# Performance work log

Hardware: AMD Instinct MI355X
Metric: run time of the kernel (lower is better)

## Reference

```python
import jax, jax.numpy as jnp
import numpy as np

N_E = 1024
E_DIM = 64
BETA = 0.25


def setup_inputs() -> dict:
    key = jax.random.key(0)
    k1, k2 = jax.random.split(key)
    z = jax.random.normal(k1, (32, 32, 32, E_DIM), dtype=jnp.float32)
    # torch init: uniform(-1/n_e, 1/n_e)
    codebook = jax.random.uniform(k2, (N_E, E_DIM), dtype=jnp.float32,
                                  minval=-1.0 / N_E, maxval=1.0 / N_E)
    return {"z": z, "codebook": codebook}


def reference(z, codebook):
    z_flat = z.reshape(-1, E_DIM)  # [N, e_dim]
    # squared euclidean distances: ||z||^2 + ||e||^2 - 2 z e^T
    d = (jnp.sum(z_flat ** 2, axis=1, keepdims=True)
         + jnp.sum(codebook ** 2, axis=1)
         - 2.0 * jnp.matmul(z_flat, codebook.T))  # [N, n_e]
    idx = jnp.argmin(d, axis=1)  # [N]
    z_q = codebook[idx].reshape(z.shape)
    sg = jax.lax.stop_gradient
    loss = jnp.mean((sg(z_q) - z) ** 2) + BETA * jnp.mean((z_q - sg(z)) ** 2)
    z_q_st = z + sg(z_q - z)  # straight-through estimator
    return z_q_st, idx, loss
```

## Files before the change

kernel.cpp:

```cpp
#include <hip/hip_runtime.h>
#include <hip/hip_bf16.h>

#define NROWS 32768
#define NE    1024
#define ED    64
#define RPB   32
#define RPW   8
#define CHUNK 256

typedef float4 f4;

__global__ __launch_bounds__(256)
void vq_main(const float* __restrict__ z, const float* __restrict__ cb,
             float* __restrict__ out, float* __restrict__ partials)
{
    __shared__ __align__(16) float zsh[RPB * ED];
    __shared__ __align__(16) float et[ED * CHUNK];
    __shared__ __align__(16) float sq[CHUNK];
    __shared__ int   idxsh[RPB];
    __shared__ float wsum[4];

    const int tid  = threadIdx.x;
    const int lane = tid & 63;
    const int w    = tid >> 6;
    const int rowbase = blockIdx.x * RPB;

    {
        const f4* zg = (const f4*)(z + (size_t)rowbase * ED);
        f4* zs = (f4*)zsh;
        zs[tid]       = zg[tid];
        zs[tid + 256] = zg[tid + 256];
    }
    __syncthreads();

    float cn[RPW];
    {
        float rj;
        {
#pragma clang fp contract(off)
            const int rl = lane >> 3;
            const int jj = lane & 7;
            const float* zr = &zsh[(w * RPW + rl) * ED];
            float a = 0.f;
#pragma unroll
            for (int i = 0; i < 8; ++i) { float v = zr[8 * i + jj]; a += v * v; }
            rj = a;
        }
        rj += __shfl_xor(rj, 1);
        rj += __shfl_xor(rj, 2);
        rj += __shfl_xor(rj, 4);
#pragma unroll
        for (int r = 0; r < RPW; ++r) cn[r] = __shfl(rj, r * 8);
    }

    float bestv[RPW];
    int   besti[RPW];
#pragma unroll
    for (int r = 0; r < RPW; ++r) { bestv[r] = INFINITY; besti[r] = 0; }

    const f4* zs4 = (const f4*)zsh;
    const f4* et4 = (const f4*)et;
    const f4* sq4 = (const f4*)sq;

    for (int ch = 0; ch < 4; ++ch) {
        __syncthreads();
        {
            const int code = ch * CHUNK + tid;
            const f4* crow = (const f4*)(cb + (size_t)code * ED);
            float v[ED];
#pragma unroll
            for (int i = 0; i < 16; ++i) {
                f4 t = crow[i];
                v[4 * i + 0] = t.x; v[4 * i + 1] = t.y;
                v[4 * i + 2] = t.z; v[4 * i + 3] = t.w;
            }
            {
#pragma clang fp contract(off)
                float r0 = v[0] * v[0], r1 = v[1] * v[1];
                float r2 = v[2] * v[2], r3 = v[3] * v[3];
                float r4 = v[4] * v[4], r5 = v[5] * v[5];
                float r6 = v[6] * v[6], r7 = v[7] * v[7];
#pragma unroll
                for (int i = 8; i < ED; i += 8) {
                    r0 += v[i + 0] * v[i + 0]; r1 += v[i + 1] * v[i + 1];
                    r2 += v[i + 2] * v[i + 2]; r3 += v[i + 3] * v[i + 3];
                    r4 += v[i + 4] * v[i + 4]; r5 += v[i + 5] * v[i + 5];
                    r6 += v[i + 6] * v[i + 6]; r7 += v[i + 7] * v[i + 7];
                }
                sq[tid] = ((r0 + r1) + (r2 + r3)) + ((r4 + r5) + (r6 + r7));
            }
#pragma unroll
            for (int i = 0; i < ED; ++i) et[i * CHUNK + tid] = v[i];
        }
        __syncthreads();

        f4 sv = sq4[lane];
        float svq[4] = {sv.x, sv.y, sv.z, sv.w};

        float acc[RPW][4];
#pragma unroll
        for (int r = 0; r < RPW; ++r)
            acc[r][0] = acc[r][1] = acc[r][2] = acc[r][3] = 0.f;

#pragma unroll 2
        for (int k4 = 0; k4 < 16; ++k4) {
            f4 e0 = et4[(4 * k4 + 0) * 64 + lane];
            f4 e1 = et4[(4 * k4 + 1) * 64 + lane];
            f4 e2 = et4[(4 * k4 + 2) * 64 + lane];
            f4 e3 = et4[(4 * k4 + 3) * 64 + lane];
#pragma unroll
            for (int r = 0; r < RPW; ++r) {
                f4 zv = zs4[(w * RPW + r) * 16 + k4];
                acc[r][0] = fmaf(zv.x, e0.x, acc[r][0]);
                acc[r][1] = fmaf(zv.x, e0.y, acc[r][1]);
                acc[r][2] = fmaf(zv.x, e0.z, acc[r][2]);
                acc[r][3] = fmaf(zv.x, e0.w, acc[r][3]);
                acc[r][0] = fmaf(zv.y, e1.x, acc[r][0]);
                acc[r][1] = fmaf(zv.y, e1.y, acc[r][1]);
                acc[r][2] = fmaf(zv.y, e1.z, acc[r][2]);
                acc[r][3] = fmaf(zv.y, e1.w, acc[r][3]);
                acc[r][0] = fmaf(zv.z, e2.x, acc[r][0]);
                acc[r][1] = fmaf(zv.z, e2.y, acc[r][1]);
                acc[r][2] = fmaf(zv.z, e2.z, acc[r][2]);
                acc[r][3] = fmaf(zv.z, e2.w, acc[r][3]);
                acc[r][0] = fmaf(zv.w, e3.x, acc[r][0]);
                acc[r][1] = fmaf(zv.w, e3.y, acc[r][1]);
                acc[r][2] = fmaf(zv.w, e3.z, acc[r][2]);
                acc[r][3] = fmaf(zv.w, e3.w, acc[r][3]);
            }
        }

        {
#pragma clang fp contract(off)
#pragma unroll
            for (int r = 0; r < RPW; ++r) {
#pragma unroll
                for (int q = 0; q < 4; ++q) {
                    float t1 = cn[r] + svq[q];
                    float d  = t1 - 2.0f * acc[r][q];
                    int j = ch * 256 + lane * 4 + q;
                    if (d < bestv[r]) { bestv[r] = d; besti[r] = j; }
                }
            }
        }
    }

    float lp = 0.f;
#pragma unroll
    for (int r = 0; r < RPW; ++r) {
        float v = bestv[r];
        int   i = besti[r];
#pragma unroll
        for (int m = 1; m < 64; m <<= 1) {
            float ov = __shfl_xor(v, m);
            int   oi = __shfl_xor(i, m);
            if (ov < v || (ov == v && oi < i)) { v = ov; i = oi; }
        }
        i &= (NE - 1);
        const int grow = rowbase + w * RPW + r;
        float zq, zz, diff, st;
        {
#pragma clang fp contract(off)
            zq   = cb[(size_t)i * ED + lane];
            zz   = zsh[(w * RPW + r) * ED + lane];
            diff = zq - zz;
            st   = zz + diff;
            lp  += diff * diff;
        }
        out[(size_t)grow * ED + lane] = st;
        if (lane == 0) idxsh[w * RPW + r] = i;
    }

#pragma unroll
    for (int m = 1; m < 64; m <<= 1) lp += __shfl_xor(lp, m);
    if (lane == 0) wsum[w] = lp;
    __syncthreads();

    if (tid < RPB) {
        int iv = idxsh[tid] & (NE - 1);
        out[(size_t)NROWS * ED + rowbase + tid] = (float)iv;
    }
    if (tid == 0)
        partials[blockIdx.x] = (wsum[0] + wsum[1]) + (wsum[2] + wsum[3]);
}

__global__ void vq_finalize(const float* __restrict__ partials,
                            float* __restrict__ out)
{
    __shared__ float red[256];
    int t = threadIdx.x;
    float s = (partials[t] + partials[t + 256]) + (partials[t + 512] + partials[t + 768]);
    red[t] = s;
    __syncthreads();
    for (int m = 128; m > 0; m >>= 1) {
        if (t < m) red[t] += red[t + m];
        __syncthreads();
    }
    if (t == 0) {
        float mean = red[0] / (float)((size_t)NROWS * ED);
        float loss = mean + 0.25f * mean;
        out[(size_t)NROWS * ED + NROWS] = loss;
    }
}

extern "C" void kernel_launch(void* const* d_in, const int* in_sizes, int n_in,
                              void* d_out, int out_size, void* d_ws, size_t ws_size,
                              hipStream_t stream)
{
    (void)in_sizes; (void)n_in; (void)out_size; (void)ws_size;
    const float* z  = (const float*)d_in[0];
    const float* cb = (const float*)d_in[1];
    float* out = (float*)d_out;
    float* partials = (float*)d_ws;

    vq_main<<<1024, 256, 0, stream>>>(z, cb, out, partials);
    vq_finalize<<<1, 256, 0, stream>>>(partials, out);
}
```

Measured before the change: 90.16 us.

## Precompute codebook norms in prep kernel and read z rows directly via scalar loads

Moves the codebook squared-norm computation into a small prep kernel run once, instead of recomputing it in each of the 1024 blocks. The main kernel no longer stages z in shared memory. It reads z rows from global memory at wave-uniform addresses, so they can become scalar loads. It also requests two blocks per CU through launch bounds. The cost is an extra kernel launch and the dependence on global or scalar cache for z reads in the inner loop.

```diff
diff --git a/kernel.cpp b/kernel.cpp
--- a/kernel.cpp
+++ b/kernel.cpp
@@ -1,56 +1,74 @@
 #include <hip/hip_runtime.h>
-#include <hip/hip_bf16.h>
 
 #define NROWS 32768
 #define NE    1024
 #define ED    64
-#define RPB   32
+#define CHUNK 256
+#define NCH   (NE / CHUNK)
 #define RPW   8
-#define CHUNK 256
 
 typedef float4 f4;
 
-__global__ __launch_bounds__(256)
+__global__ void vq_prep(const float* __restrict__ cb, float* __restrict__ ssq)
+{
+    int j = blockIdx.x * blockDim.x + threadIdx.x;
+    const f4* crow = (const f4*)(cb + (size_t)j * ED);
+    float v[ED];
+#pragma unroll
+    for (int i = 0; i < 16; ++i) {
+        f4 t = crow[i];
+        v[4*i+0] = t.x; v[4*i+1] = t.y; v[4*i+2] = t.z; v[4*i+3] = t.w;
+    }
+    {
+#pragma clang fp contract(off)
+        float r0 = v[0]*v[0], r1 = v[1]*v[1], r2 = v[2]*v[2], r3 = v[3]*v[3];
+        float r4 = v[4]*v[4], r5 = v[5]*v[5], r6 = v[6]*v[6], r7 = v[7]*v[7];
+#pragma unroll
+        for (int i = 8; i < ED; i += 8) {
+            r0 += v[i+0]*v[i+0]; r1 += v[i+1]*v[i+1];
+            r2 += v[i+2]*v[i+2]; r3 += v[i+3]*v[i+3];
+            r4 += v[i+4]*v[i+4]; r5 += v[i+5]*v[i+5];
+            r6 += v[i+6]*v[i+6]; r7 += v[i+7]*v[i+7];
+        }
+        ssq[j] = ((r0+r1)+(r2+r3)) + ((r4+r5)+(r6+r7));
+    }
+}
+
+__global__ __launch_bounds__(256, 2)
 void vq_main(const float* __restrict__ z, const float* __restrict__ cb,
-             float* __restrict__ out, float* __restrict__ partials)
-{
-    __shared__ __align__(16) float zsh[RPB * ED];
+             const float* __restrict__ ssq, float* __restrict__ out,
+             float* __restrict__ partials)
+{
     __shared__ __align__(16) float et[ED * CHUNK];
-    __shared__ __align__(16) float sq[CHUNK];
-    __shared__ int   idxsh[RPB];
+    __shared__ __align__(16) float sqsh[NE];
+    __shared__ int   idxsh[32];
     __shared__ float wsum[4];
 
     const int tid  = threadIdx.x;
     const int lane = tid & 63;
     const int w    = tid >> 6;
-    const int rowbase = blockIdx.x * RPB;
-
-    {
-        const f4* zg = (const f4*)(z + (size_t)rowbase * ED);
-        f4* zs = (f4*)zsh;
-        zs[tid]       = zg[tid];
-        zs[tid + 256] = zg[tid + 256];
-    }
-    __syncthreads();
+    const int w_u  = __builtin_amdgcn_readfirstlane(w);
+    const int rowbase = blockIdx.x * 32;
+
+    ((f4*)sqsh)[tid] = ((const f4*)ssq)[tid];
 
     float cn[RPW];
     {
-        float rj;
-        {
-#pragma clang fp contract(off)
-            const int rl = lane >> 3;
-            const int jj = lane & 7;
-            const float* zr = &zsh[(w * RPW + rl) * ED];
-            float a = 0.f;
-#pragma unroll
-            for (int i = 0; i < 8; ++i) { float v = zr[8 * i + jj]; a += v * v; }
-            rj = a;
-        }
-        rj += __shfl_xor(rj, 1);
-        rj += __shfl_xor(rj, 2);
-        rj += __shfl_xor(rj, 4);
-#pragma unroll
-        for (int r = 0; r < RPW; ++r) cn[r] = __shfl(rj, r * 8);
+        const int rl = lane >> 3;
+        const int jj = lane & 7;
+        const float* zr = z + (size_t)(rowbase + w_u * RPW + rl) * ED;
+        float a;
+        {
+#pragma clang fp contract(off)
+            a = 0.f;
+#pragma unroll
+            for (int i = 0; i < 8; ++i) { float v = zr[8*i + jj]; a += v*v; }
+        }
+        a += __shfl_xor(a, 1);
+        a += __shfl_xor(a, 2);
+        a += __shfl_xor(a, 4);
+#pragma unroll
+        for (int r = 0; r < RPW; ++r) cn[r] = __shfl(a, r * 8);
     }
 
     float bestv[RPW];
@@ -58,43 +76,25 @@
 #pragma unroll
     for (int r = 0; r < RPW; ++r) { bestv[r] = INFINITY; besti[r] = 0; }
 
-    const f4* zs4 = (const f4*)zsh;
     const f4* et4 = (const f4*)et;
-    const f4* sq4 = (const f4*)sq;
-
-    for (int ch = 0; ch < 4; ++ch) {
+    const float* zw = z + (size_t)(rowbase + w_u * RPW) * ED;
+
+    for (int ch = 0; ch < NCH; ++ch) {
         __syncthreads();
         {
-            const int code = ch * CHUNK + tid;
-            const f4* crow = (const f4*)(cb + (size_t)code * ED);
-            float v[ED];
+            const f4* crow = (const f4*)(cb + (size_t)(ch * CHUNK + tid) * ED);
 #pragma unroll
             for (int i = 0; i < 16; ++i) {
                 f4 t = crow[i];
-                v[4 * i + 0] = t.x; v[4 * i + 1] = t.y;
-                v[4 * i + 2] = t.z; v[4 * i + 3] = t.w;
+                et[(4*i+0) * CHUNK + tid] = t.x;
+                et[(4*i+1) * CHUNK + tid] = t.y;
+                et[(4*i+2) * CHUNK + tid] = t.z;
+                et[(4*i+3) * CHUNK + tid] = t.w;
             }
-            {
-#pragma clang fp contract(off)
-                float r0 = v[0] * v[0], r1 = v[1] * v[1];
-                float r2 = v[2] * v[2], r3 = v[3] * v[3];
-                float r4 = v[4] * v[4], r5 = v[5] * v[5];
-                float r6 = v[6] * v[6], r7 = v[7] * v[7];
-#pragma unroll
-                for (int i = 8; i < ED; i += 8) {
-                    r0 += v[i + 0] * v[i + 0]; r1 += v[i + 1] * v[i + 1];
-                    r2 += v[i + 2] * v[i + 2]; r3 += v[i + 3] * v[i + 3];
-                    r4 += v[i + 4] * v[i + 4]; r5 += v[i + 5] * v[i + 5];
-                    r6 += v[i + 6] * v[i + 6]; r7 += v[i + 7] * v[i + 7];
-                }
-                sq[tid] = ((r0 + r1) + (r2 + r3)) + ((r4 + r5) + (r6 + r7));
-            }
-#pragma unroll
-            for (int i = 0; i < ED; ++i) et[i * CHUNK + tid] = v[i];
         }
         __syncthreads();
 
-        f4 sv = sq4[lane];
+        f4 sv = ((const f4*)sqsh)[ch * 64 + lane];
         float svq[4] = {sv.x, sv.y, sv.z, sv.w};
 
         float acc[RPW][4];
@@ -104,30 +104,38 @@
 
 #pragma unroll 2
         for (int k4 = 0; k4 < 16; ++k4) {
-            f4 e0 = et4[(4 * k4 + 0) * 64 + lane];
-            f4 e1 = et4[(4 * k4 + 1) * 64 + lane];
-            f4 e2 = et4[(4 * k4 + 2) * 64 + lane];
-            f4 e3 = et4[(4 * k4 + 3) * 64 + lane];
-#pragma unroll
-            for (int r = 0; r < RPW; ++r) {
-                f4 zv = zs4[(w * RPW + r) * 16 + k4];
-                acc[r][0] = fmaf(zv.x, e0.x, acc[r][0]);
-                acc[r][1] = fmaf(zv.x, e0.y, acc[r][1]);
-                acc[r][2] = fmaf(zv.x, e0.z, acc[r][2]);
-                acc[r][3] = fmaf(zv.x, e0.w, acc[r][3]);
-                acc[r][0] = fmaf(zv.y, e1.x, acc[r][0]);
-                acc[r][1] = fmaf(zv.y, e1.y, acc[r][1]);
-                acc[r][2] = fmaf(zv.y, e1.z, acc[r][2]);
-                acc[r][3] = fmaf(zv.y, e1.w, acc[r][3]);
-                acc[r][0] = fmaf(zv.z, e2.x, acc[r][0]);
-                acc[r][1] = fmaf(zv.z, e2.y, acc[r][1]);
-                acc[r][2] = fmaf(zv.z, e2.z, acc[r][2]);
-                acc[r][3] = fmaf(zv.z, e2.w, acc[r][3]);
-                acc[r][0] = fmaf(zv.w, e3.x, acc[r][0]);
-                acc[r][1] = fmaf(zv.w, e3.y, acc[r][1]);
-                acc[r][2] = fmaf(zv.w, e3.z, acc[r][2]);
-                acc[r][3] = fmaf(zv.w, e3.w, acc[r][3]);
-            }
+            f4 e0 = et4[(4*k4+0) * 64 + lane];
+            f4 e1 = et4[(4*k4+1) * 64 + lane];
+            f4 e2 = et4[(4*k4+2) * 64 + lane];
+            f4 e3 = et4[(4*k4+3) * 64 + lane];
+            f4 z0 = *(const f4*)(zw + 0*ED + 4*k4);
+            f4 z1 = *(const f4*)(zw + 1*ED + 4*k4);
+            f4 z2 = *(const f4*)(zw + 2*ED + 4*k4);
+            f4 z3 = *(const f4*)(zw + 3*ED + 4*k4);
+            f4 z4 = *(const f4*)(zw + 4*ED + 4*k4);
+            f4 z5 = *(const f4*)(zw + 5*ED + 4*k4);
+            f4 z6 = *(const f4*)(zw + 6*ED + 4*k4);
+            f4 z7 = *(const f4*)(zw + 7*ED + 4*k4);
+#define ROWFMA(r, zz)                                                    \
+            acc[r][0] = fmaf(zz.x, e0.x, acc[r][0]);                     \
+            acc[r][1] = fmaf(zz.x, e0.y, acc[r][1]);                     \
+            acc[r][2] = fmaf(zz.x, e0.z, acc[r][2]);                     \
+            acc[r][3] = fmaf(zz.x, e0.w, acc[r][3]);                     \
+            acc[r][0] = fmaf(zz.y, e1.x, acc[r][0]);                     \
+            acc[r][1] = fmaf(zz.y, e1.y, acc[r][1]);                     \
+            acc[r][2] = fmaf(zz.y, e1.z, acc[r][2]);                     \
+            acc[r][3] = fmaf(zz.y, e1.w, acc[r][3]);                     \
+            acc[r][0] = fmaf(zz.z, e2.x, acc[r][0]);                     \
+            acc[r][1] = fmaf(zz.z, e2.y, acc[r][1]);                     \
+            acc[r][2] = fmaf(zz.z, e2.z, acc[r][2]);                     \
+            acc[r][3] = fmaf(zz.z, e2.w, acc[r][3]);                     \
+            acc[r][0] = fmaf(zz.w, e3.x, acc[r][0]);                     \
+            acc[r][1] = fmaf(zz.w, e3.y, acc[r][1]);                     \
+            acc[r][2] = fmaf(zz.w, e3.z, acc[r][2]);                     \
+            acc[r][3] = fmaf(zz.w, e3.w, acc[r][3]);
+            ROWFMA(0, z0) ROWFMA(1, z1) ROWFMA(2, z2) ROWFMA(3, z3)
+            ROWFMA(4, z4) ROWFMA(5, z5) ROWFMA(6, z6) ROWFMA(7, z7)
+#undef ROWFMA
         }
 
         {
@@ -138,7 +146,7 @@
                 for (int q = 0; q < 4; ++q) {
                     float t1 = cn[r] + svq[q];
                     float d  = t1 - 2.0f * acc[r][q];
-                    int j = ch * 256 + lane * 4 + q;
+                    int j = ch * CHUNK + lane * 4 + q;
                     if (d < bestv[r]) { bestv[r] = d; besti[r] = j; }
                 }
             }
@@ -162,7 +170,7 @@
         {
 #pragma clang fp contract(off)
             zq   = cb[(size_t)i * ED + lane];
-            zz   = zsh[(w * RPW + r) * ED + lane];
+            zz   = z [(size_t)grow * ED + lane];
             diff = zq - zz;
             st   = zz + diff;
             lp  += diff * diff;
@@ -176,7 +184,7 @@
     if (lane == 0) wsum[w] = lp;
     __syncthreads();
 
-    if (tid < RPB) {
+    if (tid < 32) {
         int iv = idxsh[tid] & (NE - 1);
         out[(size_t)NROWS * ED + rowbase + tid] = (float)iv;
     }
@@ -198,8 +206,7 @@
     }
     if (t == 0) {
         float mean = red[0] / (float)((size_t)NROWS * ED);
-        float loss = mean + 0.25f * mean;
-        out[(size_t)NROWS * ED + NROWS] = loss;
+        out[(size_t)NROWS * ED + NROWS] = mean + 0.25f * mean;
     }
 }
 
@@ -211,8 +218,10 @@
     const float* z  = (const float*)d_in[0];
     const float* cb = (const float*)d_in[1];
     float* out = (float*)d_out;
-    float* partials = (float*)d_ws;
-
-    vq_main<<<1024, 256, 0, stream>>>(z, cb, out, partials);
+    float* ssq      = (float*)d_ws;
+    float* partials = ssq + NE;
+
+    vq_prep<<<4, 256, 0, stream>>>(cb, ssq);
+    vq_main<<<1024, 256, 0, stream>>>(z, cb, ssq, out, partials);
     vq_finalize<<<1, 256, 0, stream>>>(partials, out);
 }
```

Result: faster. 87.80 us (-2.6%).
